# Kernel optimization log

Measured on AMD Instinct MI355X. Metric: run time of the kernel, lower is better.

## Reference

```python
import jax, jax.numpy as jnp
import numpy as np

M, B, T, C, H, HS = 2, 8, 1024, 512, 8, 64
EPS = 1e-5

NAMES = ['x','sa_kw1','sa_kb1','sa_kw2','sa_qw1','sa_qb1','sa_qw2','sa_vw1','sa_vb1','sa_vw2',
         'sa_pw1','sa_pb1','sa_pw2','sa_pb2','ff_w1','ff_b1','ff_w2','ff_b2',
         'ln1_g','ln1_b','ln2_g','ln2_b','lnc_g','lnc_b',
         'ca_qw','ca_kvw','ca_pw1','ca_pb1','ca_pw2','ca_pb2']


def setup_inputs() -> dict:
    key = jax.random.key(0)
    it = iter(jax.random.split(key, 40))
    def w(shape, s=0.02):
        return jax.random.normal(next(it), shape, jnp.float32) * s
    d = {}
    d['x'] = jax.random.normal(next(it), (M, B, T, C), jnp.float32)
    # self-attention heads: Linear(C,HS//2)+bias -> tanh -> Linear(HS//2,HS) no bias, stacked over (M,H)
    for nm in ('k', 'q', 'v'):
        d['sa_%sw1' % nm] = w((M, H, C, HS // 2))
        d['sa_%sb1' % nm] = jnp.zeros((M, H, HS // 2), jnp.float32)
        d['sa_%sw2' % nm] = w((M, H, HS // 2, HS))
    # MHA output proj: Linear(H*HS,C//2)->tanh->Linear(C//2,C)
    d['sa_pw1'] = w((M, H * HS, C // 2)); d['sa_pb1'] = jnp.zeros((M, C // 2), jnp.float32)
    d['sa_pw2'] = w((M, C // 2, C));      d['sa_pb2'] = jnp.zeros((M, C), jnp.float32)
    # feed-forward
    d['ff_w1'] = w((M, C, 4 * C)); d['ff_b1'] = jnp.zeros((M, 4 * C), jnp.float32)
    d['ff_w2'] = w((M, 4 * C, C)); d['ff_b2'] = jnp.zeros((M, C), jnp.float32)
    # layernorms
    for nm in ('ln1', 'ln2', 'lnc'):
        d[nm + '_g'] = jnp.ones((M, C), jnp.float32)
        d[nm + '_b'] = jnp.zeros((M, C), jnp.float32)
    # cross-attention: per head q proj (no bias), per-kv-modality kv proj (no bias, 2*HS)
    d['ca_qw'] = w((M, H, C, HS))
    d['ca_kvw'] = w((M, H, M - 1, C, 2 * HS))
    d['ca_pw1'] = w((M, H * HS, C // 2)); d['ca_pb1'] = jnp.zeros((M, C // 2), jnp.float32)
    d['ca_pw2'] = w((M, C // 2, C));      d['ca_pb2'] = jnp.zeros((M, C), jnp.float32)
    return d


def _ln(x, g, b):
    mu = x.mean(-1, keepdims=True)
    var = ((x - mu) ** 2).mean(-1, keepdims=True)
    return (x - mu) * jax.lax.rsqrt(var + EPS) * g + b


def _attend(q, k, v, mask):
    # q,k,v: (B,H,T,HS); causal masked softmax attention
    aff = jnp.einsum('bhtd,bhsd->bhts', q, k) * (HS ** -0.5)
    aff = jnp.where(mask, aff, -jnp.inf)
    return jnp.einsum('bhts,bhsd->bhtd', jax.nn.softmax(aff, axis=-1), v)


def _merge(o):
    # (B,H,T,HS) -> (B,T,H*HS), matching torch.cat over heads
    return o.transpose(0, 2, 1, 3).reshape(o.shape[0], o.shape[2], -1)


def _forward(p):
    mask = jnp.tril(jnp.ones((T, T), bool))
    x = p['x']
    attended = []
    for i in range(M):  # fixed small modality loop
        xi = x[i]
        h = _ln(xi, p['ln1_g'][i], p['ln1_b'][i])
        def hm(w1, b1, w2):
            # batched over heads: Linear->tanh->Linear
            z = jnp.tanh(jnp.einsum('btc,hce->bhte', h, w1) + b1[:, None, :])
            return jnp.einsum('bhte,hed->bhtd', z, w2)
        o = _attend(hm(p['sa_qw1'][i], p['sa_qb1'][i], p['sa_qw2'][i]),
                    hm(p['sa_kw1'][i], p['sa_kb1'][i], p['sa_kw2'][i]),
                    hm(p['sa_vw1'][i], p['sa_vb1'][i], p['sa_vw2'][i]), mask)
        o = jnp.tanh(_merge(o) @ p['sa_pw1'][i] + p['sa_pb1'][i]) @ p['sa_pw2'][i] + p['sa_pb2'][i]
        xi = xi + o
        h2 = _ln(xi, p['ln2_g'][i], p['ln2_b'][i])
        xi = xi + (jax.nn.relu(h2 @ p['ff_w1'][i] + p['ff_b1'][i]) @ p['ff_w2'][i] + p['ff_b2'][i])
        attended.append(xi)
    outs = []
    for i in range(M):
        xi = attended[i]
        hq = _ln(xi, p['lnc_g'][i], p['lnc_b'][i])
        q = jnp.einsum('btc,hcd->bhtd', hq, p['ca_qw'][i])
        acc = 0.0
        for jidx, j in enumerate([j for j in range(M) if j != i]):
            kv = jnp.einsum('btc,hcd->bhtd', attended[j], p['ca_kvw'][i][:, jidx])
            k, v = jnp.split(kv, 2, axis=-1)
            acc = acc + _attend(q, k, v, mask)
        o = jnp.tanh(_merge(acc) @ p['ca_pw1'][i] + p['ca_pb1'][i]) @ p['ca_pw2'][i] + p['ca_pb2'][i]
        outs.append(xi + o)
    return jnp.stack(outs)


def reference(x, sa_kw1, sa_kb1, sa_kw2, sa_qw1, sa_qb1, sa_qw2, sa_vw1, sa_vb1, sa_vw2,
              sa_pw1, sa_pb1, sa_pw2, sa_pb2, ff_w1, ff_b1, ff_w2, ff_b2,
              ln1_g, ln1_b, ln2_g, ln2_b, lnc_g, lnc_b,
              ca_qw, ca_kvw, ca_pw1, ca_pb1, ca_pw2, ca_pb2):
    args = (x, sa_kw1, sa_kb1, sa_kw2, sa_qw1, sa_qb1, sa_qw2, sa_vw1, sa_vb1, sa_vw2,
            sa_pw1, sa_pb1, sa_pw2, sa_pb2, ff_w1, ff_b1, ff_w2, ff_b2,
            ln1_g, ln1_b, ln2_g, ln2_b, lnc_g, lnc_b,
            ca_qw, ca_kvw, ca_pw1, ca_pb1, ca_pw2, ca_pb2)
    return _forward(dict(zip(NAMES, args)))
```

## Files before the change

kernel.cpp:

```cpp
#include <hip/hip_runtime.h>
#include <hip/hip_bf16.h>

#define DEVI __device__ __forceinline__

typedef __attribute__((ext_vector_type(8))) short short8v;
typedef __attribute__((ext_vector_type(4))) short short4v;
typedef __attribute__((ext_vector_type(4))) float float4v;
typedef __attribute__((ext_vector_type(16))) float f32x16;

#if defined(__has_builtin)
#if __has_builtin(__builtin_amdgcn_exp2f)
#define EXP2F(x) __builtin_amdgcn_exp2f(x)
#endif
#endif
#ifndef EXP2F
#define EXP2F(x) exp2f(x)
#endif

constexpr int Mm = 2, Bb = 8, Tt = 1024, Cc = 512, Hh = 8, HSs = 64;
constexpr int ROWS = Bb * Tt;
constexpr size_t BTC = (size_t)Bb * Tt * Cc;
constexpr size_t SLAB = (size_t)ROWS * 512;
constexpr size_t KOFF = (size_t)2 * ROWS * 768;
constexpr float SCQ = 0.18033688011112042f;

DEVI short f2bf(float f) {
    __hip_bfloat16 h = __float2bfloat16(f);
    short s; __builtin_memcpy(&s, &h, 2); return s;
}

DEVI float4v mfma16(short8v a, short8v b, float4v c) {
    return __builtin_amdgcn_mfma_f32_16x16x32_bf16(a, b, c, 0, 0, 0);
}
DEVI f32x16 mfma32(short8v a, short8v b, f32x16 c) {
    return __builtin_amdgcn_mfma_f32_32x32x16_bf16(a, b, c, 0, 0, 0);
}

DEVI void gload_lds16(const short* g, short* l) {
    __builtin_amdgcn_global_load_lds(
        (const __attribute__((address_space(1))) void*)g,
        (__attribute__((address_space(3))) void*)l, 16, 0, 0);
}

struct TDesc {
    const float* src; short* dst;
    int K, N;
    long long moff, hoff;
    int base;
};
struct TPack { TDesc d[14]; };

__global__ __launch_bounds__(256) void transpose_all(TPack p) {
    __shared__ float t[32][33];
    int bid = blockIdx.x;
    int di = 0;
#pragma unroll
    for (int i = 1; i < 14; i++) if (bid >= p.d[i].base) di = i;
    TDesc d = p.d[di];
    int local = bid - d.base;
    int kb = d.K >> 5, nb = d.N >> 5;
    int bx = local % kb; int rest = local / kb;
    int by = rest % nb;  int z = rest / nb;
    int k0 = bx * 32, n0 = by * 32;
    size_t so = (size_t)z * d.K * d.N;
    short* dst = d.dst + (size_t)(z >> 3) * d.moff + (size_t)(z & 7) * d.hoff;
    int tx = threadIdx.x & 31, ty = threadIdx.x >> 5;
#pragma unroll
    for (int i = 0; i < 32; i += 8)
        t[ty + i][tx] = d.src[so + (size_t)(k0 + ty + i) * d.N + n0 + tx];
    __syncthreads();
#pragma unroll
    for (int i = 0; i < 32; i += 8)
        dst[(size_t)(n0 + ty + i) * d.K + k0 + tx] = f2bf(t[tx][ty + i]);
}

__global__ __launch_bounds__(256) void bias_cat3(const float* __restrict__ q,
                                                 const float* __restrict__ k,
                                                 const float* __restrict__ v,
                                                 float* __restrict__ o) {
    int m = blockIdx.x, t = threadIdx.x;
    o[m * 768 + t]       = q[m * 256 + t];
    o[m * 768 + 256 + t] = k[m * 256 + t];
    o[m * 768 + 512 + t] = v[m * 256 + t];
}

__global__ __launch_bounds__(256) void ln_kernel(const float* __restrict__ x,
                                                 const float* __restrict__ g,
                                                 const float* __restrict__ b,
                                                 short* __restrict__ out, size_t xzs) {
    int z = blockIdx.y;
    x += z * xzs; g += z * Cc; b += z * Cc; out += z * SLAB;
    int row = blockIdx.x * 4 + (threadIdx.x >> 6);
    int l = threadIdx.x & 63;
    const float* xr = x + (size_t)row * Cc;
    float4 a = *(const float4*)&xr[l * 4];
    float4 c = *(const float4*)&xr[256 + l * 4];
    float s = (a.x + a.y) + (a.z + a.w) + (c.x + c.y) + (c.z + c.w);
    float q = (a.x * a.x + a.y * a.y) + (a.z * a.z + a.w * a.w) +
              (c.x * c.x + c.y * c.y) + (c.z * c.z + c.w * c.w);
#pragma unroll
    for (int o = 1; o < 64; o <<= 1) { s += __shfl_xor(s, o, 64); q += __shfl_xor(q, o, 64); }
    float mu = s * (1.f / Cc);
    float var = q * (1.f / Cc) - mu * mu;
    float rs = rsqrtf(var + 1e-5f);
    float4 ga = *(const float4*)&g[l * 4],   gc = *(const float4*)&g[256 + l * 4];
    float4 ba = *(const float4*)&b[l * 4],   bc = *(const float4*)&b[256 + l * 4];
    short4v o1, o2;
    o1[0] = f2bf((a.x - mu) * rs * ga.x + ba.x);
    o1[1] = f2bf((a.y - mu) * rs * ga.y + ba.y);
    o1[2] = f2bf((a.z - mu) * rs * ga.z + ba.z);
    o1[3] = f2bf((a.w - mu) * rs * ga.w + ba.w);
    o2[0] = f2bf((c.x - mu) * rs * gc.x + bc.x);
    o2[1] = f2bf((c.y - mu) * rs * gc.y + bc.y);
    o2[2] = f2bf((c.z - mu) * rs * gc.z + bc.z);
    o2[3] = f2bf((c.w - mu) * rs * gc.w + bc.w);
    short* orow = out + (size_t)row * Cc;
    *(short4v*)&orow[l * 4]       = o1;
    *(short4v*)&orow[256 + l * 4] = o2;
}

template<int BM, int BN, int ACT, bool BIAS, bool RES, bool WF, bool WB>
__global__ __launch_bounds__(256, 2) void gemm2(
    const short* __restrict__ A, int lda, long long a_zs,
    const short* __restrict__ Wt, int ldw, long long w_zs,
    const float* __restrict__ bias, long long bias_zs,
    const float* __restrict__ res, long long res_zs,
    float* __restrict__ outF, long long outF_zs,
    short* __restrict__ outB, long long outB_zs,
    int ldc, int K, float oscale) {
    constexpr int BK = 64;
    __shared__ short As[BM][BK];
    __shared__ short Bs[BN][BK];
    long long z = blockIdx.z;
    A += z * a_zs; Wt += z * w_zs;
    if (BIAS) bias += z * bias_zs;
    if (RES)  res  += z * res_zs;
    if (WF)   outF += z * outF_zs;
    if (WB)   outB += z * outB_zs;
    int m0 = blockIdx.x * BM, n0 = blockIdx.y * BN;
    int tid = threadIdx.x, wv = tid >> 6, l = tid & 63, lr = l & 15, lg = l >> 4;
    constexpr int WM = BM / 2, WN = BN / 2;
    int wm = wv & 1, wn = wv >> 1;
    constexpr int AI = WM / 16, BJ = WN / 16;
    float4v acc[AI][BJ] = {};
    int lrow = l >> 3;
    int gcol = (l & 7) ^ lrow;
    constexpr int CHA = BM / 8, CHB = BN / 8;
    for (int k0 = 0; k0 < K; k0 += BK) {
        __syncthreads();
#pragma unroll
        for (int c = 0; c < CHA / 4; c++) {
            int ch = wv + c * 4;
            gload_lds16(&A[(size_t)(m0 + ch * 8 + lrow) * lda + k0 + gcol * 8],
                        &As[ch * 8][0]);
        }
#pragma unroll
        for (int c = 0; c < CHB / 4; c++) {
            int ch = wv + c * 4;
            gload_lds16(&Wt[(size_t)(n0 + ch * 8 + lrow) * ldw + k0 + gcol * 8],
                        &Bs[ch * 8][0]);
        }
        __syncthreads();
#pragma unroll
        for (int kk = 0; kk < 2; kk++) {
            int g = (kk * 4 + lg) ^ (lr & 7);
            short8v af[AI], bfv[BJ];
#pragma unroll
            for (int i = 0; i < AI; i++)
                af[i] = *(const short8v*)&As[wm * WM + i * 16 + lr][g * 8];
#pragma unroll
            for (int j = 0; j < BJ; j++)
                bfv[j] = *(const short8v*)&Bs[wn * WN + j * 16 + lr][g * 8];
#pragma unroll
            for (int i = 0; i < AI; i++)
#pragma unroll
                for (int j = 0; j < BJ; j++)
                    acc[i][j] = mfma16(af[i], bfv[j], acc[i][j]);
        }
    }
#pragma unroll
    for (int i = 0; i < AI; i++) {
#pragma unroll
        for (int j = 0; j < BJ; j++) {
            int col = n0 + wn * WN + j * 16 + lr;
            float bv = BIAS ? bias[col] : 0.f;
#pragma unroll
            for (int r = 0; r < 4; r++) {
                int row = m0 + wm * WM + i * 16 + lg * 4 + r;
                float v = acc[i][j][r] * oscale + bv;
                if (ACT == 1) v = tanhf(v);
                if (ACT == 2) v = fmaxf(v, 0.f);
                size_t idx = (size_t)row * ldc + col;
                if (RES) v += res[idx];
                if (WF) outF[idx] = v;
                if (WB) outB[idx] = f2bf(v);
            }
        }
    }
}

template<int ACT, bool BIAS, bool RES, bool WF, bool WB>
__global__ __launch_bounds__(256, 2) void gemm3(
    const short* __restrict__ A, int lda, long long a_zs,
    const short* __restrict__ Wt, int ldw, long long w_zs,
    const float* __restrict__ bias, long long bias_zs,
    const float* __restrict__ res, long long res_zs,
    float* __restrict__ outF, long long outF_zs,
    short* __restrict__ outB, long long outB_zs,
    int ldc, int K, float oscale) {
    constexpr int BM = 128, BN = 128, BK = 64;
    __shared__ short As[2][BM][BK];
    __shared__ short Bs[2][BN][BK];
    long long z = blockIdx.z;
    A += z * a_zs; Wt += z * w_zs;
    if (BIAS) bias += z * bias_zs;
    if (RES)  res  += z * res_zs;
    if (WF)   outF += z * outF_zs;
    if (WB)   outB += z * outB_zs;
    int m0 = blockIdx.x * BM, n0 = blockIdx.y * BN;
    int tid = threadIdx.x, wv = tid >> 6, l = tid & 63;
    int lq = l & 31, hi = l >> 5;
    int wm = wv & 1, wn = wv >> 1;
    f32x16 acc[2][2] = {};
    int lrow = l >> 3;
    int gcol = (l & 7) ^ lrow;

    auto STAGE = [&](int bi, int k0) {
#pragma unroll
        for (int c = 0; c < 4; c++) {
            int ch = wv + c * 4;
            gload_lds16(&A[(size_t)(m0 + ch * 8 + lrow) * lda + k0 + gcol * 8],
                        &As[bi][ch * 8][0]);
        }
#pragma unroll
        for (int c = 0; c < 4; c++) {
            int ch = wv + c * 4;
            gload_lds16(&Wt[(size_t)(n0 + ch * 8 + lrow) * ldw + k0 + gcol * 8],
                        &Bs[bi][ch * 8][0]);
        }
    };

    STAGE(0, 0);
    __syncthreads();
    int NT = K / BK;
    for (int t = 0; t < NT; t++) {
        int cur = t & 1;
        if (t + 1 < NT) STAGE(cur ^ 1, (t + 1) * BK);
        const short (*Ac)[BK] = As[cur];
        const short (*Bc)[BK] = Bs[cur];
#pragma unroll
        for (int ks = 0; ks < 4; ks++) {
            int g = (ks * 2 + hi) ^ (lq & 7);
            short8v af[2], bf[2];
#pragma unroll
            for (int i = 0; i < 2; i++)
                af[i] = *(const short8v*)&Ac[wm * 64 + i * 32 + lq][g * 8];
#pragma unroll
            for (int j = 0; j < 2; j++)
                bf[j] = *(const short8v*)&Bc[wn * 64 + j * 32 + lq][g * 8];
#pragma unroll
            for (int i = 0; i < 2; i++)
#pragma unroll
                for (int j = 0; j < 2; j++)
                    acc[i][j] = mfma32(af[i], bf[j], acc[i][j]);
        }
        __syncthreads();
    }
#pragma unroll
    for (int i = 0; i < 2; i++) {
#pragma unroll
        for (int j = 0; j < 2; j++) {
            int col = n0 + wn * 64 + j * 32 + lq;
            float bv = BIAS ? bias[col] : 0.f;
#pragma unroll
            for (int r = 0; r < 16; r++) {
                int row = m0 + wm * 64 + i * 32 + 4 * hi + (r & 3) + 8 * (r >> 2);
                float v = acc[i][j][r] * oscale + bv;
                if (ACT == 1) v = tanhf(v);
                if (ACT == 2) v = fmaxf(v, 0.f);
                size_t idx = (size_t)row * ldc + col;
                if (RES) v += res[idx];
                if (WF) outF[idx] = v;
                if (WB) outB[idx] = f2bf(v);
            }
        }
    }
}

__global__ __launch_bounds__(256, 2) void gemm_kv(
    const short* __restrict__ A, long long a_zs,
    const short* __restrict__ Wt, long long w_zs,
    short* __restrict__ outB, long long outB_zs,
    short* __restrict__ VTo, int K) {
    constexpr int BK = 64;
    __shared__ short As[128][BK];
    __shared__ short Bs[128][BK];
    __shared__ short Tv[64][136];
    long long z = blockIdx.z;
    A += z * a_zs; Wt += z * w_zs; outB += z * outB_zs;
    int m0 = blockIdx.x * 128, n0 = blockIdx.y * 128;
    int tid = threadIdx.x, wv = tid >> 6, l = tid & 63, lr = l & 15, lg = l >> 4;
    int wm = wv & 1, wn = wv >> 1;
    float4v acc[4][4] = {};
    int lrow = l >> 3;
    int gcol = (l & 7) ^ lrow;
    for (int k0 = 0; k0 < K; k0 += BK) {
        __syncthreads();
#pragma unroll
        for (int c = 0; c < 4; c++) {
            int ch = wv + c * 4;
            gload_lds16(&A[(size_t)(m0 + ch * 8 + lrow) * 512 + k0 + gcol * 8],
                        &As[ch * 8][0]);
        }
#pragma unroll
        for (int c = 0; c < 4; c++) {
            int ch = wv + c * 4;
            gload_lds16(&Wt[(size_t)(n0 + ch * 8 + lrow) * 512 + k0 + gcol * 8],
                        &Bs[ch * 8][0]);
        }
        __syncthreads();
#pragma unroll
        for (int kk = 0; kk < 2; kk++) {
            int g = (kk * 4 + lg) ^ (lr & 7);
            short8v af[4], bfv[4];
#pragma unroll
            for (int i = 0; i < 4; i++)
                af[i] = *(const short8v*)&As[wm * 64 + i * 16 + lr][g * 8];
#pragma unroll
            for (int j = 0; j < 4; j++)
                bfv[j] = *(const short8v*)&Bs[wn * 64 + j * 16 + lr][g * 8];
#pragma unroll
            for (int i = 0; i < 4; i++)
#pragma unroll
                for (int j = 0; j < 4; j++)
                    acc[i][j] = mfma16(af[i], bfv[j], acc[i][j]);
        }
    }
    if (wn == 0) {
#pragma unroll
        for (int i = 0; i < 4; i++)
#pragma unroll
            for (int j = 0; j < 4; j++) {
                int col = n0 + j * 16 + lr;
#pragma unroll
                for (int r = 0; r < 4; r++) {
                    int row = m0 + wm * 64 + i * 16 + lg * 4 + r;
                    outB[(size_t)row * 1024 + col] = f2bf(acc[i][j][r]);
                }
            }
    } else {
#pragma unroll
        for (int i = 0; i < 4; i++)
#pragma unroll
            for (int j = 0; j < 4; j++) {
                int d = j * 16 + lr;
#pragma unroll
                for (int r = 0; r < 4; r++)
                    Tv[d][wm * 64 + i * 16 + lg * 4 + r] = f2bf(acc[i][j][r]);
            }
    }
    __syncthreads();
    int b = m0 >> 10, trow0 = m0 & 1023, h = n0 >> 7;
    short* dst = VTo + (size_t)(blockIdx.z * 64 + b * 8 + h) * 65536;
    int d = tid >> 2, c0 = (tid & 3) * 32;
#pragma unroll
    for (int q = 0; q < 4; q++)
        *(short8v*)&dst[(size_t)d * Tt + trow0 + c0 + q * 8] =
            *(const short8v*)&Tv[d][c0 + q * 8];
}

__global__ __launch_bounds__(256) void proj2(const short* __restrict__ Z,
                                             const short* __restrict__ W2,
                                             short* __restrict__ Qo,
                                             short* __restrict__ Ko,
                                             short* __restrict__ VTo,
                                             float qscale) {
    __shared__ short As[64][40], Ws[64][40];
    __shared__ short Tv[64][72];
    int zz = blockIdx.y, t = zz >> 4, m = (zz >> 3) & 1, h = zz & 7;
    int m0 = blockIdx.x * 64;
    const short* Ap = Z + (size_t)m * ((size_t)ROWS * 768) + t * 256 + h * 32;
    const short* Wp = W2 + (size_t)zz * 2048;
    float sc = (t == 0) ? qscale : 1.0f;
    int tid = threadIdx.x, w = tid >> 6, l = tid & 63, lr = l & 15, lg = l >> 4;
    int r = tid >> 2, c = (tid & 3) * 8;
    *(short8v*)&As[r][c] = *(const short8v*)&Ap[(size_t)(m0 + r) * 768 + c];
    *(short8v*)&Ws[r][c] = *(const short8v*)&Wp[r * 32 + c];
    __syncthreads();
    short8v af = *(const short8v*)&As[w * 16 + lr][lg * 8];
    float4v acc[4] = {};
#pragma unroll
    for (int j = 0; j < 4; j++) {
        short8v bf = *(const short8v*)&Ws[j * 16 + lr][lg * 8];
        acc[j] = mfma16(af, bf, acc[j]);
    }
    if (t < 2) {
        short* Op = (t == 0 ? Qo : Ko) + (size_t)m * SLAB + h * 64;
#pragma unroll
        for (int j = 0; j < 4; j++)
#pragma unroll
            for (int rr = 0; rr < 4; rr++)
                Op[(size_t)(m0 + w * 16 + lg * 4 + rr) * 512 + j * 16 + lr] =
                    f2bf(acc[j][rr] * sc);
    } else {
#pragma unroll
        for (int j = 0; j < 4; j++)
#pragma unroll
            for (int rr = 0; rr < 4; rr++)
                Tv[j * 16 + lr][w * 16 + lg * 4 + rr] = f2bf(acc[j][rr]);
        __syncthreads();
        int b = m0 >> 10, trow0 = m0 & 1023;
        int z64 = m * 64 + b * 8 + h;
        short* dst = VTo + (size_t)z64 * 65536;
        int d = w * 16 + (l >> 2), toff = (l & 3) * 16;
        *(short8v*)&dst[(size_t)d * Tt + trow0 + toff]     = *(const short8v*)&Tv[d][toff];
        *(short8v*)&dst[(size_t)d * Tt + trow0 + toff + 8] = *(const short8v*)&Tv[d][toff + 8];
    }
}

__global__ __launch_bounds__(512, 4) void flash_attn4(
    const short* __restrict__ Q, const short* __restrict__ K,
    const short* __restrict__ VT, short* __restrict__ O,
    int krs, int khs, long long qzs, long long kzs, long long vtzs, long long ozs)
{
    __shared__ short Ks[2][64][64];
    __shared__ short Vs[2][64][64];
    int id = blockIdx.x;
    int bh = id & 63, mod = (id >> 6) & 1, p = (id >> 7) & 3;
    Q += (long long)mod * qzs; K += (long long)mod * kzs;
    VT += (long long)mod * vtzs; O += (long long)mod * ozs;
    int b = bh >> 3, h = bh & 7;
    int tid = threadIdx.x, w = tid >> 6, l = tid & 63;
    int lq = l & 31, hi = l >> 5;
    int strip = (w < 4) ? p : 7 - p;
    int qwb = strip * 128 + (w & 3) * 32;
    int qabs = qwb + lq;
    const short* Qp = Q + (size_t)b * Tt * Cc + h * HSs;
    const short* Kp = K + (size_t)b * Tt * krs + h * khs;
    const short* Vp = VT + (size_t)bh * HSs * Tt;
    short* Op = O + (size_t)b * Tt * Cc + h * HSs;

    short8v qf[4];
#pragma unroll
    for (int c = 0; c < 4; c++)
        qf[c] = *(const short8v*)&Qp[(size_t)qabs * Cc + (c * 2 + hi) * 8];

    f32x16 oacc[2] = {};
    float mrun = -1e30f, lrun = 0.f;
    int nk = 2 * (7 - p) + 2;
    short8v pk, pv;

    auto LOADT = [&](int kb) {
        int r = tid >> 3, cg = (tid & 7) ^ (r & 7);
        pk = *(const short8v*)&Kp[(size_t)(kb + r) * krs + cg * 8];
        pv = *(const short8v*)&Vp[(size_t)r * Tt + kb + cg * 8];
    };
    auto STORET = [&](int bi) {
        int r = tid >> 3, cp = tid & 7;
        *(short8v*)&Ks[bi][r][cp * 8] = pk;
        *(short8v*)&Vs[bi][r][cp * 8] = pv;
    };

    LOADT(0); STORET(0); __syncthreads();

    for (int t = 0; t < nk; t++) {
        int cur = t & 1, kb = t * 64;
        bool pre = (t + 1 < nk);
        if (pre) LOADT(kb + 64);
        if (kb <= qwb + 31) {
            bool full = (kb + 63 <= qwb);
            f32x16 st[2] = {};
            __builtin_amdgcn_s_setprio(1);
#pragma unroll
            for (int kh = 0; kh < 2; kh++) {
#pragma unroll
                for (int cc = 0; cc < 4; cc++) {
                    int r = kh * 32 + lq;
                    int cp = (cc * 2 + hi) ^ (r & 7);
                    short8v af = *(const short8v*)&Ks[cur][r][cp * 8];
                    st[kh] = mfma32(af, qf[cc], st[kh]);
                }
            }
            __builtin_amdgcn_s_setprio(0);
            float pr[32];
            if (full) {
#pragma unroll
                for (int kh = 0; kh < 2; kh++)
#pragma unroll
                    for (int r = 0; r < 16; r++) pr[kh * 16 + r] = st[kh][r];
            } else {
#pragma unroll
                for (int kh = 0; kh < 2; kh++)
#pragma unroll
                    for (int r = 0; r < 16; r++) {
                        int kabs = kb + kh * 32 + (r & 3) + 8 * (r >> 2) + 4 * hi;
                        pr[kh * 16 + r] = (kabs <= qabs) ? st[kh][r] : -3.0e38f;
                    }
            }
            float t16[16];
#pragma unroll
            for (int i = 0; i < 16; i++) t16[i] = fmaxf(pr[i], pr[i + 16]);
#pragma unroll
            for (int i = 0; i < 8; i++) t16[i] = fmaxf(t16[i], t16[i + 8]);
            float mx = fmaxf(fmaxf(fmaxf(t16[0], t16[4]), fmaxf(t16[1], t16[5])),
                             fmaxf(fmaxf(t16[2], t16[6]), fmaxf(t16[3], t16[7])));
            mx = fmaxf(mx, __shfl_xor(mx, 32));
            if (!__all(mx <= mrun + 11.5f)) {
                float mn = fmaxf(mrun, mx);
                float al = EXP2F(mrun - mn);
                mrun = mn;
                lrun *= al;
#pragma unroll
                for (int dh = 0; dh < 2; dh++)
#pragma unroll
                    for (int r = 0; r < 16; r++) oacc[dh][r] *= al;
            }
#pragma unroll
            for (int i = 0; i < 32; i++) pr[i] = EXP2F(pr[i] - mrun);
            float s16[16];
#pragma unroll
            for (int i = 0; i < 16; i++) s16[i] = pr[i] + pr[i + 16];
#pragma unroll
            for (int i = 0; i < 8; i++) s16[i] = s16[i] + s16[i + 8];
            float rsum = ((s16[0] + s16[4]) + (s16[1] + s16[5])) +
                         ((s16[2] + s16[6]) + (s16[3] + s16[7]));
            rsum += __shfl_xor(rsum, 32);
            lrun += rsum;
#pragma unroll
            for (int ks = 0; ks < 4; ks++) {
                unsigned x0, x1, y0, y1;
                asm("v_cvt_pk_bf16_f32 %0, %1, %2" : "=v"(x0) : "v"(pr[ks*8+0]), "v"(pr[ks*8+1]));
                asm("v_cvt_pk_bf16_f32 %0, %1, %2" : "=v"(x1) : "v"(pr[ks*8+2]), "v"(pr[ks*8+3]));
                asm("v_cvt_pk_bf16_f32 %0, %1, %2" : "=v"(y0) : "v"(pr[ks*8+4]), "v"(pr[ks*8+5]));
                asm("v_cvt_pk_bf16_f32 %0, %1, %2" : "=v"(y1) : "v"(pr[ks*8+6]), "v"(pr[ks*8+7]));
                asm volatile("v_permlane32_swap_b32 %0, %1" : "+v"(x0), "+v"(y0));
                asm volatile("v_permlane32_swap_b32 %0, %1" : "+v"(x1), "+v"(y1));
                union { unsigned u[4]; short8v s; } uu;
                uu.u[0] = x0; uu.u[1] = x1; uu.u[2] = y0; uu.u[3] = y1;
                __builtin_amdgcn_s_setprio(1);
#pragma unroll
                for (int dh = 0; dh < 2; dh++) {
                    int r = dh * 32 + lq;
                    int cp = (ks * 2 + hi) ^ (r & 7);
                    short8v vf = *(const short8v*)&Vs[cur][r][cp * 8];
                    oacc[dh] = mfma32(vf, uu.s, oacc[dh]);
                }
                __builtin_amdgcn_s_setprio(0);
            }
        }
        if (pre) STORET(cur ^ 1);
        __syncthreads();
    }
    float inv = 1.f / lrun;
#pragma unroll
    for (int dh = 0; dh < 2; dh++)
#pragma unroll
        for (int r = 0; r < 16; r += 2) {
            unsigned wds;
            float a0 = oacc[dh][r] * inv, a1 = oacc[dh][r + 1] * inv;
            asm("v_cvt_pk_bf16_f32 %0, %1, %2" : "=v"(wds) : "v"(a0), "v"(a1));
            int d = (r & 3) + 8 * (r >> 2) + 4 * hi + dh * 32;
            *(unsigned*)&Op[(size_t)qabs * Cc + d] = wds;
        }
}

extern "C" void kernel_launch(void* const* d_in, const int* in_sizes, int n_in,
                              void* d_out, int out_size, void* d_ws, size_t ws_size,
                              hipStream_t stream) {
    (void)in_sizes; (void)n_in; (void)out_size; (void)ws_size;
    const float* X     = (const float*)d_in[0];
    const float* saKW1 = (const float*)d_in[1];
    const float* saKB1 = (const float*)d_in[2];
    const float* saKW2 = (const float*)d_in[3];
    const float* saQW1 = (const float*)d_in[4];
    const float* saQB1 = (const float*)d_in[5];
    const float* saQW2 = (const float*)d_in[6];
    const float* saVW1 = (const float*)d_in[7];
    const float* saVB1 = (const float*)d_in[8];
    const float* saVW2 = (const float*)d_in[9];
    const float* saPW1 = (const float*)d_in[10];
    const float* saPB1 = (const float*)d_in[11];
    const float* saPW2 = (const float*)d_in[12];
    const float* saPB2 = (const float*)d_in[13];
    const float* ffW1  = (const float*)d_in[14];
    const float* ffB1  = (const float*)d_in[15];
    const float* ffW2  = (const float*)d_in[16];
    const float* ffB2  = (const float*)d_in[17];
    const float* ln1g  = (const float*)d_in[18];
    const float* ln1b  = (const float*)d_in[19];
    const float* ln2g  = (const float*)d_in[20];
    const float* ln2b  = (const float*)d_in[21];
    const float* lncg  = (const float*)d_in[22];
    const float* lncb  = (const float*)d_in[23];
    const float* caQW  = (const float*)d_in[24];
    const float* caKVW = (const float*)d_in[25];
    const float* caPW1 = (const float*)d_in[26];
    const float* caPB1 = (const float*)d_in[27];
    const float* caPW2 = (const float*)d_in[28];
    const float* caPB2 = (const float*)d_in[29];
    float* OUT = (float*)d_out;

    char* ws = (char*)d_ws;
    size_t cur = 0;
    auto alloc = [&](size_t bytes) -> char* {
        char* p = ws + cur; cur += (bytes + 255) & ~(size_t)255; return p;
    };

    short* WT = (short*)alloc((size_t)7700480 * 2);
    size_t wo = 0;
    auto wslot = [&](size_t e) -> short* { short* p = WT + wo; wo += e; return p; };
    short* w_qkv1 = wslot(786432);
    short* w_qkv2 = wslot(98304);
    short* w_pw1 = wslot(262144); short* w_pw2 = wslot(262144);
    short* w_ff1 = wslot(2097152); short* w_ff2 = wslot(2097152);
    short* w_caq = wslot(524288);  short* w_cakv = wslot(1048576);
    short* w_cp1 = wslot(262144);  short* w_cp2 = wslot(262144);
    float* bqkv = (float*)alloc(2 * 768 * 4);

    short* Hb  = (short*)alloc(2 * SLAB * 2);
    short* Qb  = (short*)alloc(2 * SLAB * 2);
    short* Obf = (short*)alloc(2 * SLAB * 2);
    short* Fb  = (short*)alloc((size_t)2 * ROWS * 2048 * 2);
    short* AB  = (short*)alloc(2 * SLAB * 2);
    short* VTb = Hb;
    short* P1b = Hb;
    short* Kb = Fb + KOFF;

    TPack tp;
    int base = 0, ti = 0;
    auto addT = [&](const float* s, short* d, int K, int N, int slices,
                    long long moff, long long hoff) {
        tp.d[ti++] = TDesc{s, d, K, N, moff, hoff, base};
        base += (K / 32) * (N / 32) * slices;
    };
    addT(saQW1, w_qkv1,          512, 32, 16, 393216, 16384);
    addT(saKW1, w_qkv1 + 131072, 512, 32, 16, 393216, 16384);
    addT(saVW1, w_qkv1 + 262144, 512, 32, 16, 393216, 16384);
    addT(saQW2, w_qkv2,          32, 64, 16, 16384, 2048);
    addT(saKW2, w_qkv2 + 32768,  32, 64, 16, 16384, 2048);
    addT(saVW2, w_qkv2 + 65536,  32, 64, 16, 16384, 2048);
    addT(saPW1, w_pw1, 512, 256, 2, 0, 131072);
    addT(saPW2, w_pw2, 256, 512, 2, 0, 131072);
    addT(ffW1,  w_ff1, 512, 2048, 2, 0, 1048576);
    addT(ffW2,  w_ff2, 2048, 512, 2, 0, 1048576);
    addT(caQW,  w_caq, 512, 64, 16, 262144, 32768);
    addT(caKVW, w_cakv, 512, 128, 16, 524288, 65536);
    addT(caPW1, w_cp1, 512, 256, 2, 0, 131072);
    addT(caPW2, w_cp2, 256, 512, 2, 0, 131072);
    transpose_all<<<dim3(base), 256, 0, stream>>>(tp);
    bias_cat3<<<2, 256, 0, stream>>>(saQB1, saKB1, saVB1, bqkv);

    ln_kernel<<<dim3(ROWS / 4, 2), 256, 0, stream>>>(X, ln1g, ln1b, Hb, BTC);
    gemm2<128, 128, 1, true, false, false, true><<<dim3(64, 6, 2), 256, 0, stream>>>(
        Hb, 512, SLAB, w_qkv1, 512, 393216, bqkv, 768,
        nullptr, 0, nullptr, 0, Fb, (long long)ROWS * 768, 768, 512, 1.0f);
    proj2<<<dim3(128, 48), 256, 0, stream>>>(Fb, w_qkv2, Qb, Kb, VTb, SCQ);
    flash_attn4<<<dim3(512), 512, 0, stream>>>(
        Qb, Kb, VTb, Obf, 512, 64, SLAB, SLAB, 4194304, SLAB);
    gemm2<64, 128, 1, true, false, false, true><<<dim3(128, 2, 2), 256, 0, stream>>>(
        Obf, 512, SLAB, w_pw1, 512, 131072, saPB1, 256,
        nullptr, 0, nullptr, 0, P1b, (long long)ROWS * 256, 256, 512, 1.0f);
    gemm2<64, 128, 0, true, true, true, false><<<dim3(128, 4, 2), 256, 0, stream>>>(
        P1b, 256, (long long)ROWS * 256, w_pw2, 256, 131072, saPB2, 512,
        X, BTC, OUT, BTC, nullptr, 0, 512, 256, 1.0f);
    ln_kernel<<<dim3(ROWS / 4, 2), 256, 0, stream>>>(OUT, ln2g, ln2b, Hb, BTC);
    gemm2<128, 128, 2, true, false, false, true><<<dim3(64, 16, 2), 256, 0, stream>>>(
        Hb, 512, SLAB, w_ff1, 512, 1048576, ffB1, 2048,
        nullptr, 0, nullptr, 0, Fb, (long long)ROWS * 2048, 2048, 512, 1.0f);
    gemm3<0, true, true, true, true><<<dim3(64, 4, 2), 256, 0, stream>>>(
        Fb, 2048, (long long)ROWS * 2048, w_ff2, 2048, 1048576, ffB2, 512,
        OUT, BTC, OUT, BTC, AB, SLAB, 512, 2048, 1.0f);

    ln_kernel<<<dim3(ROWS / 4, 2), 256, 0, stream>>>(OUT, lncg, lncb, Hb, BTC);
    gemm2<64, 128, 0, false, false, false, true><<<dim3(128, 4, 2), 256, 0, stream>>>(
        Hb, 512, SLAB, w_caq, 512, 262144, nullptr, 0,
        nullptr, 0, nullptr, 0, Qb, SLAB, 512, 512, SCQ);
    gemm_kv<<<dim3(64, 8, 2), 256, 0, stream>>>(
        AB + SLAB, -(long long)SLAB, w_cakv, 524288,
        Fb, (long long)ROWS * 1024, VTb, 512);
    flash_attn4<<<dim3(512), 512, 0, stream>>>(
        Qb, Fb, VTb, Obf, 1024, 128, SLAB, (long long)ROWS * 1024, 4194304, SLAB);
    gemm2<64, 128, 1, true, false, false, true><<<dim3(128, 2, 2), 256, 0, stream>>>(
        Obf, 512, SLAB, w_cp1, 512, 131072, caPB1, 256,
        nullptr, 0, nullptr, 0, P1b, (long long)ROWS * 256, 256, 512, 1.0f);
    gemm2<64, 128, 0, true, true, true, false><<<dim3(128, 4, 2), 256, 0, stream>>>(
        P1b, 256, (long long)ROWS * 256, w_cp2, 256, 131072, caPB2, 512,
        OUT, BTC, OUT, BTC, nullptr, 0, 512, 256, 1.0f);
}
```

Baseline: 348.0 us.

## Pipeline GEMM loads with vmcnt waits, reuse gemm5 for big GEMMs, bf16 LN inputs

Renames gemm3 to gemm5 and replaces its __syncthreads with explicit s_waitcnt vmcnt counts plus raw s_barrier. The intent is to let the next tile's global-to-LDS loads stay in flight while the current tile is computed. The QKV1 and FF1 GEMMs now use this 128x128 double-buffered kernel instead of gemm2. The residual GEMMs also write a bf16 copy, and a new ln_bf kernel reads that copy, so LayerNorm loads half the bytes. In exchange, LN statistics come from bf16-rounded values, and the hand-tuned vmcnt count must match the eight loads issued per stage.

After: 370.2 us. 1.06x slower.

```diff
diff --git a/kernel.cpp b/kernel.cpp
--- a/kernel.cpp
+++ b/kernel.cpp
@@ -27,6 +27,10 @@
 DEVI short f2bf(float f) {
     __hip_bfloat16 h = __float2bfloat16(f);
     short s; __builtin_memcpy(&s, &h, 2); return s;
+}
+DEVI float bf2f(short s) {
+    unsigned u = ((unsigned)(unsigned short)s) << 16;
+    float f; __builtin_memcpy(&f, &u, 4); return f;
 }
 
 DEVI float4v mfma16(short8v a, short8v b, float4v c) {
@@ -117,6 +121,37 @@
     short* orow = out + (size_t)row * Cc;
     *(short4v*)&orow[l * 4]       = o1;
     *(short4v*)&orow[256 + l * 4] = o2;
+}
+
+__global__ __launch_bounds__(256) void ln_bf(const short* __restrict__ x,
+                                             const float* __restrict__ g,
+                                             const float* __restrict__ b,
+                                             short* __restrict__ out) {
+    int z = blockIdx.y;
+    x += z * SLAB; g += z * Cc; b += z * Cc; out += z * SLAB;
+    int row = blockIdx.x * 4 + (threadIdx.x >> 6);
+    int l = threadIdx.x & 63;
+    const short* xr = x + (size_t)row * Cc;
+    short8v v = *(const short8v*)&xr[l * 8];
+    float xv[8];
+    float s = 0.f, q = 0.f;
+#pragma unroll
+    for (int i = 0; i < 8; i++) {
+        xv[i] = bf2f(v[i]);
+        s += xv[i]; q += xv[i] * xv[i];
+    }
+#pragma unroll
+    for (int o = 1; o < 64; o <<= 1) { s += __shfl_xor(s, o, 64); q += __shfl_xor(q, o, 64); }
+    float mu = s * (1.f / Cc);
+    float var = q * (1.f / Cc) - mu * mu;
+    float rs = rsqrtf(var + 1e-5f);
+    short8v ov;
+#pragma unroll
+    for (int i = 0; i < 8; i++) {
+        float gg = g[l * 8 + i], bb = b[l * 8 + i];
+        ov[i] = f2bf((xv[i] - mu) * rs * gg + bb);
+    }
+    *(short8v*)&out[(size_t)row * Cc + l * 8] = ov;
 }
 
 template<int BM, int BN, int ACT, bool BIAS, bool RES, bool WF, bool WB>
@@ -200,7 +235,7 @@
 }
 
 template<int ACT, bool BIAS, bool RES, bool WF, bool WB>
-__global__ __launch_bounds__(256, 2) void gemm3(
+__global__ __launch_bounds__(256, 2) void gemm5(
     const short* __restrict__ A, int lda, long long a_zs,
     const short* __restrict__ Wt, int ldw, long long w_zs,
     const float* __restrict__ bias, long long bias_zs,
@@ -241,11 +276,17 @@
     };
 
     STAGE(0, 0);
-    __syncthreads();
     int NT = K / BK;
     for (int t = 0; t < NT; t++) {
         int cur = t & 1;
-        if (t + 1 < NT) STAGE(cur ^ 1, (t + 1) * BK);
+        if (t + 1 < NT) {
+            STAGE(cur ^ 1, (t + 1) * BK);
+            asm volatile("s_waitcnt vmcnt(8)" ::: "memory");
+        } else {
+            asm volatile("s_waitcnt vmcnt(0)" ::: "memory");
+        }
+        __builtin_amdgcn_sched_barrier(0);
+        __builtin_amdgcn_s_barrier();
         const short (*Ac)[BK] = As[cur];
         const short (*Bc)[BK] = Bs[cur];
 #pragma unroll
@@ -264,7 +305,8 @@
                 for (int j = 0; j < 2; j++)
                     acc[i][j] = mfma32(af[i], bf[j], acc[i][j]);
         }
-        __syncthreads();
+        __builtin_amdgcn_sched_barrier(0);
+        __builtin_amdgcn_s_barrier();
     }
 #pragma unroll
     for (int i = 0; i < 2; i++) {
@@ -651,7 +693,7 @@
     bias_cat3<<<2, 256, 0, stream>>>(saQB1, saKB1, saVB1, bqkv);
 
     ln_kernel<<<dim3(ROWS / 4, 2), 256, 0, stream>>>(X, ln1g, ln1b, Hb, BTC);
-    gemm2<128, 128, 1, true, false, false, true><<<dim3(64, 6, 2), 256, 0, stream>>>(
+    gemm5<1, true, false, false, true><<<dim3(64, 6, 2), 256, 0, stream>>>(
         Hb, 512, SLAB, w_qkv1, 512, 393216, bqkv, 768,
         nullptr, 0, nullptr, 0, Fb, (long long)ROWS * 768, 768, 512, 1.0f);
     proj2<<<dim3(128, 48), 256, 0, stream>>>(Fb, w_qkv2, Qb, Kb, VTb, SCQ);
@@ -660,18 +702,18 @@
     gemm2<64, 128, 1, true, false, false, true><<<dim3(128, 2, 2), 256, 0, stream>>>(
         Obf, 512, SLAB, w_pw1, 512, 131072, saPB1, 256,
         nullptr, 0, nullptr, 0, P1b, (long long)ROWS * 256, 256, 512, 1.0f);
-    gemm2<64, 128, 0, true, true, true, false><<<dim3(128, 4, 2), 256, 0, stream>>>(
+    gemm2<64, 128, 0, true, true, true, true><<<dim3(128, 4, 2), 256, 0, stream>>>(
         P1b, 256, (long long)ROWS * 256, w_pw2, 256, 131072, saPB2, 512,
-        X, BTC, OUT, BTC, nullptr, 0, 512, 256, 1.0f);
-    ln_kernel<<<dim3(ROWS / 4, 2), 256, 0, stream>>>(OUT, ln2g, ln2b, Hb, BTC);
-    gemm2<128, 128, 2, true, false, false, true><<<dim3(64, 16, 2), 256, 0, stream>>>(
+        X, BTC, OUT, BTC, Obf, SLAB, 512, 256, 1.0f);
+    ln_bf<<<dim3(ROWS / 4, 2), 256, 0, stream>>>(Obf, ln2g, ln2b, Hb);
+    gemm5<2, true, false, false, true><<<dim3(64, 16, 2), 256, 0, stream>>>(
         Hb, 512, SLAB, w_ff1, 512, 1048576, ffB1, 2048,
         nullptr, 0, nullptr, 0, Fb, (long long)ROWS * 2048, 2048, 512, 1.0f);
-    gemm3<0, true, true, true, true><<<dim3(64, 4, 2), 256, 0, stream>>>(
+    gemm5<0, true, true, true, true><<<dim3(64, 4, 2), 256, 0, stream>>>(
         Fb, 2048, (long long)ROWS * 2048, w_ff2, 2048, 1048576, ffB2, 512,
         OUT, BTC, OUT, BTC, AB, SLAB, 512, 2048, 1.0f);
 
-    ln_kernel<<<dim3(ROWS / 4, 2), 256, 0, stream>>>(OUT, lncg, lncb, Hb, BTC);
+    ln_bf<<<dim3(ROWS / 4, 2), 256, 0, stream>>>(AB, lncg, lncb, Hb);
     gemm2<64, 128, 0, false, false, false, true><<<dim3(128, 4, 2), 256, 0, stream>>>(
         Hb, 512, SLAB, w_caq, 512, 262144, nullptr, 0,
         nullptr, 0, nullptr, 0, Qb, SLAB, 512, 512, SCQ);
```
